# Kernel optimization log

Hardware: AMD Instinct MI355X
Metric: run time of the kernel (lower is better)

The kernel has to match this reference:

```python
import jax, jax.numpy as jnp
import numpy as np

C_IN, D_MODEL = 7, 128
B, TOTAL_LEN, VALID_LEN = 32, 1024, 768
D_TOT = C_IN * D_MODEL  # 896


def setup_inputs() -> dict:
    key = jax.random.key(0)
    k1, k2, k3, k4 = jax.random.split(key, 4)
    x = jax.random.normal(k1, (B, C_IN, TOTAL_LEN), dtype=jnp.float32)
    # all rows share the same valid prefix length (required by the module's assert)
    mask = jnp.broadcast_to(jnp.arange(TOTAL_LEN)[None, :] < VALID_LEN, (B, TOTAL_LEN))
    # grouped 1x1 conv weight: [c_in*d_model, 1, 1] -> per-channel scale vector [C_IN, D_MODEL]
    w_lift = jax.random.normal(k2, (C_IN, D_MODEL), dtype=jnp.float32) * 0.1
    # RoutingModule q/k projections (identity-init + noise, as in H-Net)
    eye = jnp.eye(D_TOT, dtype=jnp.float32)
    w_q = eye + 0.02 * jax.random.normal(k3, (D_TOT, D_TOT), dtype=jnp.float32)
    w_k = eye + 0.02 * jax.random.normal(k4, (D_TOT, D_TOT), dtype=jnp.float32)
    return {"x": x, "mask": mask, "w_lift": w_lift, "w_q": w_q, "w_k": w_k}


def _normalize(v):
    n = jnp.linalg.norm(v, axis=-1, keepdims=True)
    return v / jnp.maximum(n, 1e-12)


def reference(x, mask, w_lift, w_q, w_k):
    Bq, C, T = x.shape
    # grouped 1x1 conv (kernel=1) == per-channel outer product with w_lift;
    # conv on valid prefix then zero-pad == conv on full length * mask (pointwise kernel)
    lifted = (x[:, :, None, :] * w_lift[None, :, :, None]).reshape(Bq, C * D_MODEL, T)
    lifted = lifted * mask[:, None, :].astype(lifted.dtype)
    h = jnp.transpose(lifted, (0, 2, 1))  # [B, T, D_tot]

    # ---- RoutingModule: cosine similarity of adjacent projected tokens ----
    q = _normalize(h[:, :-1] @ w_q.T)   # [B, T-1, D]
    k = _normalize(h[:, 1:] @ w_k.T)    # [B, T-1, D]
    cos_sim = jnp.sum(q * k, axis=-1)   # [B, T-1]
    p = jnp.clip((1.0 - cos_sim) * 0.5, 0.0, 1.0)
    p = jnp.pad(p, ((0, 0), (1, 0)), constant_values=1.0)  # first token is always a boundary
    boundary_prob = jnp.stack([1.0 - p, p], axis=-1)        # [B, T, 2]
    boundary_mask = (p > 0.5) & mask                        # [B, T] bool

    # ---- ChunkLayer: compact boundary tokens to the front (stable argsort gather) ----
    tok_idx = jnp.arange(T)[None, :] + (~boundary_mask).astype(jnp.int32) * T
    order = jnp.argsort(tok_idx, axis=1)                    # boundary tokens first, in order
    gathered = jnp.take_along_axis(h, order[:, :, None], axis=1)  # [B, T, D_tot]
    num_tokens = jnp.sum(boundary_mask, axis=-1)            # [B]
    chunked_mask = jnp.arange(T)[None, :] < num_tokens[:, None]   # [B, T]
    gathered = gathered * chunked_mask[:, :, None].astype(gathered.dtype)

    # rearrange 'b n (c d) -> (b c) n d'
    chunked = gathered.reshape(Bq, T, C, D_MODEL).transpose(0, 2, 1, 3).reshape(Bq * C, T, D_MODEL)
    # dropout is identity in eval mode
    return chunked, boundary_mask, boundary_prob, chunked_mask
```

## Files before the change

### kernel.cpp

```cpp
#include <hip/hip_runtime.h>

#define B_  32
#define C_  7
#define T_  1024
#define V_  768
#define D_  128
#define DT_ 896

#define OFF_BM ((size_t)B_*C_*T_*D_)
#define OFF_BP (OFF_BM + (size_t)B_*T_)
#define OFF_CM (OFF_BP + (size_t)B_*T_*2)


__global__ void qk_vecs(const float* __restrict__ wq, const float* __restrict__ wk,
                        const float* __restrict__ wl,
                        double* __restrict__ Q, double* __restrict__ K) {
    int gid = blockIdx.x * 256 + threadIdx.x;
    if (gid >= 2 * C_ * DT_) return;
    int which = gid / (C_ * DT_);
    int r = gid - which * (C_ * DT_);
    int c = r / DT_;
    int i = r - c * DT_;
    const float* W = which ? wk : wq;
    const float* wrow = W + (size_t)i * DT_ + c * D_;
    const float* wlc = wl + c * D_;
    double s = 0.0;
    #pragma unroll 8
    for (int d = 0; d < D_; ++d) s += (double)wrow[d] * (double)wlc[d];
    (which ? K : Q)[c * DT_ + i] = s;
}

__global__ void gram(const double* __restrict__ Q, const double* __restrict__ K,
                     double* __restrict__ G) {
    int blk = blockIdx.x;
    int g = blk / 49;
    int pr = blk % 49;
    int c = pr / 7, c2 = pr % 7;
    const double* a = (g == 1) ? K : Q;
    const double* b = (g == 0) ? Q : K;
    double s = 0.0;
    for (int i = threadIdx.x; i < DT_; i += 256) s += a[c * DT_ + i] * b[c2 * DT_ + i];
    __shared__ double red[256];
    red[threadIdx.x] = s;
    __syncthreads();
    for (int o = 128; o > 0; o >>= 1) {
        if (threadIdx.x < o) red[threadIdx.x] += red[threadIdx.x + o];
        __syncthreads();
    }
    if (threadIdx.x == 0) G[blk] = red[0];
}

__global__ __launch_bounds__(1024) void router(const float* __restrict__ x,
                                               const double* __restrict__ G,
                                               float* __restrict__ out,
                                               int* __restrict__ idx,
                                               int* __restrict__ num) {
    const int b = blockIdx.x, t = threadIdx.x;
    __shared__ float xs[C_][T_];
    __shared__ double Gs[147];
    __shared__ int wtot[16];
    for (int c = 0; c < C_; ++c) xs[c][t] = x[((size_t)b * C_ + c) * T_ + t];
    if (t < 147) Gs[t] = G[t];
    __syncthreads();

    double xt[C_], xp[C_];
    const bool vt = (t < V_);
    const bool vp = (t >= 1) && (t <= V_);
    #pragma unroll
    for (int c = 0; c < C_; ++c) {
        xt[c] = vt ? (double)xs[c][t] : 0.0;
        xp[c] = vp ? (double)xs[c][t - 1] : 0.0;
    }

    double p;
    if (t == 0) {
        p = 1.0;
    } else {
        double A = 0.0, Bv = 0.0, Dv = 0.0;
        #pragma unroll
        for (int c = 0; c < C_; ++c) {
            const double xpc = xp[c], xtc = xt[c];
            #pragma unroll
            for (int c2 = 0; c2 < C_; ++c2) {
                A  += xpc * xp[c2] * Gs[0 * 49 + c * 7 + c2];
                Bv += xtc * xt[c2] * Gs[1 * 49 + c * 7 + c2];
                Dv += xpc * xt[c2] * Gs[2 * 49 + c * 7 + c2];
            }
        }
        const double qn = fmax(sqrt(A), 1e-12);
        const double kn = fmax(sqrt(Bv), 1e-12);
        const double cosv = Dv / (qn * kn);
        p = fmin(fmax((1.0 - cosv) * 0.5, 0.0), 1.0);
    }
    const bool bound = (p > 0.5) && (t < V_);

    out[OFF_BM + (size_t)b * T_ + t] = bound ? 1.0f : 0.0f;
    out[OFF_BP + ((size_t)b * T_ + t) * 2 + 0] = (float)(1.0 - p);
    out[OFF_BP + ((size_t)b * T_ + t) * 2 + 1] = (float)p;

    const unsigned long long mb = __ballot(bound);
    const int lane = t & 63, wv = t >> 6;
    if (lane == 0) wtot[wv] = __popcll(mb);
    __syncthreads();
    const int before = __popcll(mb & ((1ull << lane) - 1ull));
    int offs = 0, total = 0;
    #pragma unroll
    for (int w = 0; w < 16; ++w) {
        const int v = wtot[w];
        if (w < wv) offs += v;
        total += v;
    }
    if (bound) idx[b * T_ + offs + before] = t;
    out[OFF_CM + (size_t)b * T_ + t] = (t < total) ? 1.0f : 0.0f;
    if (t == 0) num[b] = total;
}

__global__ void scatter(const float* __restrict__ x, const float* __restrict__ wl,
                        const int* __restrict__ idx, const int* __restrict__ num,
                        float4* __restrict__ out4) {
    const int i4 = blockIdx.x * 256 + threadIdx.x;
    const int d4 = i4 & 31;
    const int n  = (i4 >> 5) & (T_ - 1);
    const int bc = i4 >> 15;
    const int c = bc % 7, b = bc / 7;
    float4 v = make_float4(0.f, 0.f, 0.f, 0.f);
    if (n < num[b]) {
        const int t = idx[b * T_ + n];
        const float s = x[((size_t)b * C_ + c) * T_ + t];
        const float4 w = ((const float4*)wl)[c * 32 + d4];
        v = make_float4(s * w.x, s * w.y, s * w.z, s * w.w);
    }
    out4[i4] = v;
}

extern "C" void kernel_launch(void* const* d_in, const int* in_sizes, int n_in,
                              void* d_out, int out_size, void* d_ws, size_t ws_size,
                              hipStream_t stream) {
    const float* x  = (const float*)d_in[0];
    const float* wl = (const float*)d_in[2];
    const float* wq = (const float*)d_in[3];
    const float* wk = (const float*)d_in[4];
    float* out = (float*)d_out;

    double* wsd = (double*)d_ws;
    double* Q = wsd;
    double* K = wsd + C_ * DT_;
    double* G = wsd + 2 * C_ * DT_;
    int* idx = (int*)(wsd + 12800);
    int* num = idx + B_ * T_;

    qk_vecs<<<49, 256, 0, stream>>>(wq, wk, wl, Q, K);
    gram<<<147, 256, 0, stream>>>(Q, K, G);
    router<<<B_, 1024, 0, stream>>>(x, G, out, idx, num);
    scatter<<<28672, 256, 0, stream>>>(x, wl, idx, num, (float4*)out);
}
```

Before: 147.2 us.

## Fuse Q/K projection and Gram kernels; use nontemporal stores in scatter

Merges the qk_vecs and gram kernels into one prep kernel in which each of the 147 blocks recomputes the projected vectors it needs directly from w_q/w_k, saving one launch and the round trip through workspace. The price is redundant work: every block re-reads 896x128 weight slices for both operands, which multiplies weight traffic and double-precision FMAs by about 7x. The scatter kernel writes its large output with nontemporal stores and uses a simplified block/thread index mapping.

```diff
diff --git a/kernel.cpp b/kernel.cpp
--- a/kernel.cpp
+++ b/kernel.cpp
@@ -11,35 +11,32 @@
 #define OFF_BP (OFF_BM + (size_t)B_*T_)
 #define OFF_CM (OFF_BP + (size_t)B_*T_*2)
 
+typedef float f32x4 __attribute__((ext_vector_type(4)));
 
-__global__ void qk_vecs(const float* __restrict__ wq, const float* __restrict__ wk,
-                        const float* __restrict__ wl,
-                        double* __restrict__ Q, double* __restrict__ K) {
-    int gid = blockIdx.x * 256 + threadIdx.x;
-    if (gid >= 2 * C_ * DT_) return;
-    int which = gid / (C_ * DT_);
-    int r = gid - which * (C_ * DT_);
-    int c = r / DT_;
-    int i = r - c * DT_;
-    const float* W = which ? wk : wq;
-    const float* wrow = W + (size_t)i * DT_ + c * D_;
-    const float* wlc = wl + c * D_;
+__global__ void prep(const float* __restrict__ wq, const float* __restrict__ wk,
+                     const float* __restrict__ wl, double* __restrict__ G) {
+    const int blk = blockIdx.x;
+    const int g = blk / 49, pr = blk % 49;
+    const int ca = pr / 7, cb = pr % 7;
+    const float* Wa = (g == 1) ? wk : wq;
+    const float* Wb = (g == 0) ? wq : wk;
+    __shared__ double wla[D_], wlb[D_];
+    if (threadIdx.x < D_)            wla[threadIdx.x]       = (double)wl[ca * D_ + threadIdx.x];
+    else if (threadIdx.x < 2 * D_)   wlb[threadIdx.x - D_]  = (double)wl[cb * D_ + threadIdx.x - D_];
+    __syncthreads();
+
     double s = 0.0;
-    #pragma unroll 8
-    for (int d = 0; d < D_; ++d) s += (double)wrow[d] * (double)wlc[d];
-    (which ? K : Q)[c * DT_ + i] = s;
-}
-
-__global__ void gram(const double* __restrict__ Q, const double* __restrict__ K,
-                     double* __restrict__ G) {
-    int blk = blockIdx.x;
-    int g = blk / 49;
-    int pr = blk % 49;
-    int c = pr / 7, c2 = pr % 7;
-    const double* a = (g == 1) ? K : Q;
-    const double* b = (g == 0) ? Q : K;
-    double s = 0.0;
-    for (int i = threadIdx.x; i < DT_; i += 256) s += a[c * DT_ + i] * b[c2 * DT_ + i];
+    for (int i = threadIdx.x; i < DT_; i += 256) {
+        const float* ra = Wa + (size_t)i * DT_ + ca * D_;
+        const float* rb = Wb + (size_t)i * DT_ + cb * D_;
+        double qa = 0.0, qb = 0.0;
+        #pragma unroll 8
+        for (int d = 0; d < D_; ++d) {
+            qa += (double)ra[d] * wla[d];
+            qb += (double)rb[d] * wlb[d];
+        }
+        s += qa * qb;
+    }
     __shared__ double red[256];
     red[threadIdx.x] = s;
     __syncthreads();
@@ -110,27 +107,31 @@
         if (w < wv) offs += v;
         total += v;
     }
-    if (bound) idx[b * T_ + offs + before] = t;
+    if (bound) idx[(b << 10) + offs + before] = t;
     out[OFF_CM + (size_t)b * T_ + t] = (t < total) ? 1.0f : 0.0f;
     if (t == 0) num[b] = total;
 }
 
-__global__ void scatter(const float* __restrict__ x, const float* __restrict__ wl,
-                        const int* __restrict__ idx, const int* __restrict__ num,
-                        float4* __restrict__ out4) {
-    const int i4 = blockIdx.x * 256 + threadIdx.x;
-    const int d4 = i4 & 31;
-    const int n  = (i4 >> 5) & (T_ - 1);
-    const int bc = i4 >> 15;
+__global__ __launch_bounds__(256) void scatter(const float* __restrict__ x,
+                                               const f32x4* __restrict__ wl4,
+                                               const int* __restrict__ idx,
+                                               const int* __restrict__ num,
+                                               f32x4* __restrict__ out4) {
+    const int blk = blockIdx.x;
+    const int tid = threadIdx.x;
+    const int bc = blk >> 7;
     const int c = bc % 7, b = bc / 7;
-    float4 v = make_float4(0.f, 0.f, 0.f, 0.f);
-    if (n < num[b]) {
-        const int t = idx[b * T_ + n];
-        const float s = x[((size_t)b * C_ + c) * T_ + t];
-        const float4 w = ((const float4*)wl)[c * 32 + d4];
-        v = make_float4(s * w.x, s * w.y, s * w.z, s * w.w);
+    const int n = ((blk & 127) << 3) + (tid >> 5);
+    const int d4 = tid & 31;
+    const int nb = num[b];
+    f32x4 v = {0.f, 0.f, 0.f, 0.f};
+    if (n < nb) {
+        const int t = idx[(b << 10) + n];
+        const float s = x[(size_t)((b * 7 + c) << 10) + t];
+        const f32x4 w = wl4[c * 32 + d4];
+        v = s * w;
     }
-    out4[i4] = v;
+    __builtin_nontemporal_store(v, &out4[(size_t)blk * 256 + tid]);
 }
 
 extern "C" void kernel_launch(void* const* d_in, const int* in_sizes, int n_in,
@@ -143,14 +144,11 @@
     float* out = (float*)d_out;
 
     double* wsd = (double*)d_ws;
-    double* Q = wsd;
-    double* K = wsd + C_ * DT_;
-    double* G = wsd + 2 * C_ * DT_;
-    int* idx = (int*)(wsd + 12800);
+    double* G = wsd;
+    int* idx = (int*)(wsd + 256);
     int* num = idx + B_ * T_;
 
-    qk_vecs<<<49, 256, 0, stream>>>(wq, wk, wl, Q, K);
-    gram<<<147, 256, 0, stream>>>(Q, K, G);
+    prep<<<147, 256, 0, stream>>>(wq, wk, wl, G);
     router<<<B_, 1024, 0, stream>>>(x, G, out, idx, num);
-    scatter<<<28672, 256, 0, stream>>>(x, wl, idx, num, (float4*)out);
+    scatter<<<28672, 256, 0, stream>>>(x, (const f32x4*)wl, idx, num, (f32x4*)out);
 }
```

New measurement: 176.6 us. 1.2x slower.
